# Optimization experiments

Hardware: AMD Instinct MI355X
Metric: run time of the kernel (lower is better)

Reference implementation:

```python
import jax, jax.numpy as jnp
import numpy as np

H_LSTM = 100
FORGET_BIAS = 1.0  # TF LSTMCell default


def conv2d(x, w, b, relu=True):
    # x: [N,H,W,Cin], w: [kh,kw,Cin,Cout]
    y = jax.lax.conv_general_dilated(
        x, w, window_strides=(1, 1), padding='SAME',
        dimension_numbers=('NHWC', 'HWIO', 'NHWC')) + b
    return jax.nn.relu(y) if relu else y


def lstm(xs, W, b):
    # xs: [T, N, D]; W: [D+H, 4H] with TF gate order (i, j, f, o); b: [4H]
    N = xs.shape[1]
    H = W.shape[1] // 4
    c0 = jnp.zeros((N, H), xs.dtype)
    h0 = jnp.zeros((N, H), xs.dtype)

    def step(carry, x_t):
        c, h = carry
        z = jnp.concatenate([x_t, h], axis=-1) @ W + b
        i, j, f, o = jnp.split(z, 4, axis=-1)
        c = jax.nn.sigmoid(f + FORGET_BIAS) * c + jax.nn.sigmoid(i) * jnp.tanh(j)
        h = jax.nn.sigmoid(o) * jnp.tanh(c)
        return (c, h), h

    _, hs = jax.lax.scan(step, (c0, h0), xs)
    return hs  # [T, N, H]


def setup_inputs() -> dict:
    B, L, C = 64, 55, 24
    key = jax.random.key(0)
    ks = jax.random.split(key, 32)
    s = 0.05
    inp = {'x': jax.random.normal(ks[0], (B, 13, 13, L, C), jnp.float32)}
    # 1x1 conv block (p1)
    cins = [C, 30, 30, 30]
    for i in range(4):
        inp[f'w1{i}'] = jax.random.normal(ks[1 + i], (1, 1, cins[i], 30), jnp.float32) * s
        inp[f'b1{i}'] = jnp.zeros((30,), jnp.float32)
    # 5x5 conv block (p2)
    for i in range(4):
        inp[f'w2{i}'] = jax.random.normal(ks[5 + i], (5, 5, 30, 30), jnp.float32) * s
        inp[f'b2{i}'] = jnp.zeros((30,), jnp.float32)
    # LSTM layers: inputs 30 -> 100 and 100 -> 100
    inp['lstm1_w'] = jax.random.uniform(ks[9], (30 + H_LSTM, 4 * H_LSTM), jnp.float32, -0.1, 0.1)
    inp['lstm1_b'] = jnp.zeros((4 * H_LSTM,), jnp.float32)
    inp['lstm2_w'] = jax.random.uniform(ks[10], (H_LSTM + H_LSTM, 4 * H_LSTM), jnp.float32, -0.1, 0.1)
    inp['lstm2_b'] = jnp.zeros((4 * H_LSTM,), jnp.float32)
    # final 1x1 conv, no activation
    inp['we'] = jax.random.normal(ks[11], (1, 1, H_LSTM, 1), jnp.float32) * s
    inp['be'] = jnp.zeros((1,), jnp.float32)
    return inp


def reference(x, w10, b10, w11, b11, w12, b12, w13, b13,
              w20, b20, w21, b21, w22, b22, w23, b23,
              lstm1_w, lstm1_b, lstm2_w, lstm2_b, we, be):
    B, _, _, L, C = x.shape
    # [B,13,13,L,C] -> [L,B,13,13,C] -> [L*B,13,13,C]
    h = jnp.transpose(x, (3, 0, 1, 2, 4)).reshape(L * B, 13, 13, C)
    for w, b in ((w10, b10), (w11, b11), (w12, b12), (w13, b13),
                 (w20, b20), (w21, b21), (w22, b22), (w23, b23)):
        h = conv2d(h, w, b, relu=True)
    # time-major sequence: [L, B*13*13, 30]
    h = h.reshape(L, B * 13 * 13, 30)
    h = lstm(h, lstm1_w, lstm1_b)
    h = lstm(h, lstm2_w, lstm2_b)
    h = h.reshape(L * B, 13, 13, H_LSTM)
    h = conv2d(h, we, be, relu=False)  # [L*B,13,13,1]
    h = h.reshape(L, B, 13, 13)
    return jnp.transpose(h, (1, 2, 3, 0))  # [B,13,13,L]
```

## Files before the change

kernel.cpp:

```cpp
#include <hip/hip_runtime.h>
#include <math.h>

#define N_ROWS 10816
#define T_SEQ 55
#define NPIX 169

__device__ __forceinline__ float fast_rcp(float x){
    return __builtin_amdgcn_rcpf(x);
}
__device__ __forceinline__ float fast_sig(float x){
    return fast_rcp(1.0f + __expf(-x));
}
__device__ __forceinline__ float fast_tanh(float x){
    float ax = fabsf(x);
    float e  = __expf(-2.0f*ax);
    float r  = (1.0f - e)*fast_rcp(1.0f + e);
    return copysignf(r, x);
}

typedef __attribute__((ext_vector_type(8))) _Float16 hfrag;
typedef __attribute__((ext_vector_type(4))) float facc;

__global__ __launch_bounds__(256) void repack_conv_f16(
    const float* __restrict__ w20, const float* __restrict__ w21,
    const float* __restrict__ w22, const float* __restrict__ w23,
    _Float16* __restrict__ cw)
{
    int i = blockIdx.x*256 + threadIdx.x;
    if (i >= 4*25600) return;
    int layer = i / 25600, r = i - layer*25600;
    int frag = r >> 9, e = r & 511;
    int kt = frag >> 1, ct = frag & 1;
    int lane = e >> 3, j = e & 7;
    int ci = ((lane>>4)<<3) + j;
    int co = ct*16 + (lane & 15);
    const float* w = (layer==0)?w20:(layer==1)?w21:(layer==2)?w22:w23;
    float v = (ci<30 && co<30) ? w[(size_t)(kt*30 + ci)*30 + co] : 0.f;
    cw[i] = (_Float16)v;
}

__global__ __launch_bounds__(256, 4) void conv_fused(
    const float* __restrict__ x,
    const float* __restrict__ w0, const float* __restrict__ b0,
    const float* __restrict__ w1, const float* __restrict__ b1,
    const float* __restrict__ w2, const float* __restrict__ b2,
    const float* __restrict__ w3, const float* __restrict__ b3,
    const _Float16* __restrict__ cw,
    const float* __restrict__ cb0, const float* __restrict__ cb1,
    const float* __restrict__ cb2, const float* __restrict__ cb3,
    float* __restrict__ buf)
{
    __shared__ __align__(16) _Float16 img[18*17*32];

    int bi = blockIdx.x;
    int l = bi >> 6, b = bi & 63;
    float* ip = buf + (size_t)l*30*N_ROWS + (size_t)b*NPIX;
    const int tid = threadIdx.x;
    const int wave = tid >> 6, lane = tid & 63;
    const int m16 = lane & 15, quad = lane >> 4;

    for (int i=tid; i<18*17*16; i+=256) ((unsigned*)img)[i] = 0u;
    __syncthreads();

    if (tid < NPIX){
        const float* xp = x + ((size_t)(b*NPIX + tid)*T_SEQ + l)*24;
        float in24[24];
        #pragma unroll
        for (int i=0;i<6;i++){
            float4 v = *(const float4*)(xp + 4*i);
            in24[4*i]=v.x; in24[4*i+1]=v.y; in24[4*i+2]=v.z; in24[4*i+3]=v.w;
        }
        float a[30], c[30];
        #pragma unroll
        for (int co=0;co<30;co++) a[co]=b0[co];
        #pragma unroll
        for (int ci=0;ci<24;ci++){
            float v = in24[ci];
            #pragma unroll
            for (int co=0;co<30;co++) a[co] = fmaf(v, w0[ci*30+co], a[co]);
        }
        #pragma unroll
        for (int co=0;co<30;co++) a[co] = fmaxf(a[co],0.f);

#define LAYER30(wp, bp) \
        { _Pragma("unroll") for (int co=0;co<30;co++) c[co]=(bp)[co]; \
          _Pragma("unroll") for (int ci=0;ci<30;ci++){ float v=a[ci]; \
            _Pragma("unroll") for (int co=0;co<30;co++) c[co]=fmaf(v,(wp)[ci*30+co],c[co]); } \
          _Pragma("unroll") for (int co=0;co<30;co++) a[co]=fmaxf(c[co],0.f); }

        LAYER30(w1,b1);
        LAYER30(w2,b2);
        LAYER30(w3,b3);
#undef LAYER30

        int py = tid/13, px = tid - py*13;
        int L = (py+2)*17 + (px+2);
        #pragma unroll
        for (int ci=0;ci<30;ci++)
            img[L*32 + ((((ci>>3) + L)&3)<<3) + (ci&7)] = (_Float16)a[ci];
    }

    int pL[3]; bool mv[3];
    #pragma unroll
    for (int mi=0; mi<3; mi++){
        int Mt = wave + mi*4;
        mv[mi] = (Mt < 11);
        int p = Mt*16 + m16;
        int py = p/13, px = p - py*13;
        pL[mi] = py*17 + px;
    }

    #pragma unroll 1
    for (int layer=0; layer<4; layer++){
        const float* bias = (layer==0)?cb0:(layer==1)?cb1:(layer==2)?cb2:cb3;
        const _Float16* wh = cw + (size_t)layer*25600;

        __syncthreads();

        float bb[2];
        #pragma unroll
        for (int nt=0; nt<2; nt++){
            int co = nt*16 + m16;
            bb[nt] = (co < 30) ? bias[co] : 0.f;
        }
        facc acc[3][2];
        #pragma unroll
        for (int mi=0; mi<3; mi++)
            #pragma unroll
            for (int nt=0; nt<2; nt++)
                acc[mi][nt] = (facc){bb[nt], bb[nt], bb[nt], bb[nt]};

        #pragma unroll 1
        for (int kt=0; kt<25; kt++){
            int dy = kt/5, dx = kt - dy*5;
            int Ld = dy*17 + dx;
            hfrag ah[3];
            #pragma unroll
            for (int mi=0; mi<3; mi++){
                if (mv[mi]){
                    int L = pL[mi] + Ld;
                    int o = L*32 + (((quad + L)&3)<<3);
                    ah[mi] = *(const hfrag*)(img + o);
                }
            }
            const _Float16* whp = wh + (size_t)(kt*2)*512 + lane*8;
            hfrag wh0 = *(const hfrag*)(whp);
            hfrag wh1 = *(const hfrag*)(whp + 512);
            #pragma unroll
            for (int mi=0; mi<3; mi++){
                if (mv[mi]){
                    acc[mi][0] = __builtin_amdgcn_mfma_f32_16x16x32_f16(ah[mi], wh0, acc[mi][0],0,0,0);
                    acc[mi][1] = __builtin_amdgcn_mfma_f32_16x16x32_f16(ah[mi], wh1, acc[mi][1],0,0,0);
                }
            }
        }

        __syncthreads();

        if (layer < 3){
            #pragma unroll
            for (int mi=0; mi<3; mi++){
                if (mv[mi]){
                    int Mt = wave + mi*4;
                    #pragma unroll
                    for (int nt=0; nt<2; nt++){
                        int co = nt*16 + m16;
                        if (co < 30){
                            #pragma unroll
                            for (int i2=0; i2<4; i2++){
                                int p = Mt*16 + quad*4 + i2;
                                if (p < NPIX){
                                    float v = fmaxf(acc[mi][nt][i2], 0.f);
                                    int py = p/13, px = p - py*13;
                                    int L = (py+2)*17 + (px+2);
                                    img[L*32 + ((((co>>3) + L)&3)<<3) + (co&7)] = (_Float16)v;
                                }
                            }
                        }
                    }
                }
            }
        } else {
            #pragma unroll
            for (int mi=0; mi<3; mi++){
                if (mv[mi]){
                    int Mt = wave + mi*4;
                    #pragma unroll
                    for (int nt=0; nt<2; nt++){
                        int co = nt*16 + m16;
                        if (co < 30){
                            #pragma unroll
                            for (int i2=0; i2<4; i2++){
                                int p = Mt*16 + quad*4 + i2;
                                if (p < NPIX)
                                    ip[(size_t)co*N_ROWS + p] = fmaxf(acc[mi][nt][i2], 0.f);
                            }
                        }
                    }
                }
            }
        }
    }
}

__global__ __launch_bounds__(256) void repack_mfma_f16(
    const float* __restrict__ l1w, const float* __restrict__ l1b,
    const float* __restrict__ l2w, const float* __restrict__ l2b,
    _Float16* __restrict__ bw1, _Float16* __restrict__ bw2,
    float* __restrict__ pbias1, float* __restrict__ pbias2)
{
    const int S1 = 5*32*512;
    const int S2 = 7*32*512;
    int i = blockIdx.x*256 + threadIdx.x;
    if (i < S1){
        int fr = i >> 9, r = i & 511;
        int kt = fr >> 5, ct = fr & 31;
        int lane = r >> 3, j = r & 7;
        int k = kt*32 + ((lane>>4)<<3) + j;
        int n = lane & 15;
        int cell = ((ct>>2)<<4) + n, g = ct & 3;
        float w = (k<130 && cell<100) ? l1w[(size_t)k*400 + g*100 + cell] : 0.f;
        bw1[i] = (_Float16)w;
    } else if (i < S1 + S2){
        int ii = i - S1;
        int fr = ii >> 9, r = ii & 511;
        int kt = fr >> 5, ct = fr & 31;
        int lane = r >> 3, j = r & 7;
        int k = kt*32 + ((lane>>4)<<3) + j;
        int n = lane & 15;
        int cell = ((ct>>2)<<4) + n, g = ct & 3;
        float w = (k<200 && cell<100) ? l2w[(size_t)k*400 + g*100 + cell] : 0.f;
        bw2[ii] = (_Float16)w;
    } else if (i < S1+S2+512){
        int col = i - S1 - S2;
        int ct = col >> 4, n = col & 15;
        int cell = ((ct>>2)<<4) + n, g = ct & 3;
        pbias1[col] = (cell<100) ? l1b[g*100+cell] : 0.f;
    } else if (i < S1+S2+1024){
        int col = i - S1 - S2 - 512;
        int ct = col >> 4, n = col & 15;
        int cell = ((ct>>2)<<4) + n, g = ct & 3;
        pbias2[col] = (cell<100) ? l2b[g*100+cell] : 0.f;
    }
}

#define NKT1 5
#define NKT2 7
#define M_BLK 32
#define RSTR 40
#define KTSTR (32*RSTR)
__global__ __launch_bounds__(512, 4) void lstm_mfma11(
    const float* __restrict__ xall,
    const _Float16* __restrict__ bw1, const _Float16* __restrict__ bw2,
    const float* __restrict__ pbias1, const float* __restrict__ pbias2,
    const float* __restrict__ we, const float* __restrict__ be,
    float* __restrict__ out)
{
    __shared__ __align__(16) _Float16 A1[NKT1*KTSTR];
    __shared__ __align__(16) _Float16 A2[NKT2*KTSTR];
    __shared__ float pbuf[8*M_BLK];

    const int tid  = threadIdx.x;
    const int w    = tid >> 6, lane = tid & 63;
    const int m16  = lane & 15, quad = lane >> 4;
    const int n0   = blockIdx.x * M_BLK;
    const int cell = w*16 + m16;
    const bool cv  = (cell < 100);

    for (int i=tid; i<NKT1*KTSTR; i+=512) A1[i]=(_Float16)0.f;
    for (int i=tid; i<NKT2*KTSTR; i+=512) A2[i]=(_Float16)0.f;
    for (int i=tid; i<8*M_BLK; i+=512) pbuf[i]=0.f;

    float cs1[2][4] = {{0,0,0,0},{0,0,0,0}};
    float cs2[2][4] = {{0,0,0,0},{0,0,0,0}};
    float b1[4], b2[4];
    #pragma unroll
    for (int g=0; g<4; g++){
        b1[g] = pbias1[(w*4+g)*16 + m16];
        b2[g] = pbias2[(w*4+g)*16 + m16];
    }
    const float weC = cv ? we[cell] : 0.f;
    const float be0 = be[0];

    const _Float16* w1p = bw1 + ((size_t)(w*4)*64 + lane)*8;
    const _Float16* w2p = bw2 + ((size_t)(w*4)*64 + lane)*8;

    const int sk = tid >> 3, sq = tid & 7;

    __syncthreads();

    if (tid < 240){
        float4 v = *(const float4*)(xall + (size_t)sk*N_ROWS + n0 + sq*4);
        A1[(sq*4+0)*RSTR + sk] = (_Float16)v.x;
        A1[(sq*4+1)*RSTR + sk] = (_Float16)v.y;
        A1[(sq*4+2)*RSTR + sk] = (_Float16)v.z;
        A1[(sq*4+3)*RSTR + sk] = (_Float16)v.w;
    }
    __syncthreads();

    facc acc[2][4];

#define GEMM(W0, NKT, AH, BI) \
    { _Pragma("unroll") \
      for (int mt=0; mt<2; mt++) \
        _Pragma("unroll") \
        for (int g=0; g<4; g++){ float bb=(BI)[g]; acc[mt][g]=(facc){bb,bb,bb,bb}; } \
      _Pragma("unroll 1") \
      for (int kt=0; kt<(NKT); kt++){ \
        hfrag ah[2]; \
        _Pragma("unroll") \
        for (int mt=0; mt<2; mt++){ \
            int off = kt*KTSTR + (mt*16+m16)*RSTR + (quad<<3); \
            ah[mt] = *(const hfrag*)((AH) + off); } \
        const _Float16* whp = (W0) + (size_t)kt*16384; \
        hfrag wh[4]; \
        _Pragma("unroll") \
        for (int g=0; g<4; g++) wh[g] = *(const hfrag*)(whp + (size_t)g*512); \
        _Pragma("unroll") \
        for (int g=0; g<4; g++){ \
            acc[0][g]=__builtin_amdgcn_mfma_f32_16x16x32_f16(ah[0],wh[g],acc[0][g],0,0,0); \
            acc[1][g]=__builtin_amdgcn_mfma_f32_16x16x32_f16(ah[1],wh[g],acc[1][g],0,0,0); } \
      } }

    for (int t=0; t<T_SEQ; t++){
        float4 xn;
        if (t+1 < T_SEQ && tid < 240)
            xn = *(const float4*)(xall + ((size_t)(t+1)*30+sk)*N_ROWS + n0 + sq*4);

        GEMM(w1p, NKT1, A1, b1);
        __syncthreads();

        if (cv){
            #pragma unroll
            for (int mt=0; mt<2; mt++){
                #pragma unroll
                for (int i2=0;i2<4;i2++){
                    float gi = fast_sig(acc[mt][0][i2]);
                    float gj = fast_tanh(acc[mt][1][i2]);
                    float gf = fast_sig(acc[mt][2][i2] + 1.0f);
                    float go = fast_sig(acc[mt][3][i2]);
                    float cn = gf*cs1[mt][i2] + gi*gj;
                    cs1[mt][i2] = cn;
                    float h = go*fast_tanh(cn);
                    int row = mt*16 + quad*4 + i2;
                    _Float16 hh = (_Float16)h;
                    int k1 = 30 + cell;
                    A1[(k1>>5)*KTSTR + row*RSTR + (k1&31)] = hh;
                    A2[(cell>>5)*KTSTR + row*RSTR + (cell&31)] = hh;
                }
            }
        }
        if (t+1 < T_SEQ && tid < 240){
            A1[(sq*4+0)*RSTR + sk] = (_Float16)xn.x;
            A1[(sq*4+1)*RSTR + sk] = (_Float16)xn.y;
            A1[(sq*4+2)*RSTR + sk] = (_Float16)xn.z;
            A1[(sq*4+3)*RSTR + sk] = (_Float16)xn.w;
        }
        __syncthreads();

        GEMM(w2p, NKT2, A2, b2);
        __syncthreads();

        if (w < 7){
            float pp[2][4] = {{0,0,0,0},{0,0,0,0}};
            if (cv){
                #pragma unroll
                for (int mt=0; mt<2; mt++){
                    #pragma unroll
                    for (int i2=0;i2<4;i2++){
                        float gi = fast_sig(acc[mt][0][i2]);
                        float gj = fast_tanh(acc[mt][1][i2]);
                        float gf = fast_sig(acc[mt][2][i2] + 1.0f);
                        float go = fast_sig(acc[mt][3][i2]);
                        float cn = gf*cs2[mt][i2] + gi*gj;
                        cs2[mt][i2] = cn;
                        float h = go*fast_tanh(cn);
                        pp[mt][i2] = h*weC;
                        int row = mt*16 + quad*4 + i2;
                        int k1 = 100 + cell;
                        A2[(k1>>5)*KTSTR + row*RSTR + (k1&31)] = (_Float16)h;
                    }
                }
            }
            #pragma unroll
            for (int mt=0; mt<2; mt++){
                #pragma unroll
                for (int i2=0;i2<4;i2++){
                    float p = pp[mt][i2];
                    p += __shfl_xor(p, 1);
                    p += __shfl_xor(p, 2);
                    p += __shfl_xor(p, 4);
                    p += __shfl_xor(p, 8);
                    pp[mt][i2] = p;
                }
            }
            if (m16 == 0){
                #pragma unroll
                for (int mt=0; mt<2; mt++)
                    #pragma unroll
                    for (int i2=0;i2<4;i2++)
                        pbuf[w*M_BLK + mt*16 + quad*4 + i2] = pp[mt][i2];
            }
        }
        __syncthreads();

        if (tid < M_BLK){
            float s = be0;
            #pragma unroll
            for (int ww=0; ww<8; ww++) s += pbuf[ww*M_BLK + tid];
            out[(size_t)(n0+tid)*T_SEQ + t] = s;
        }
    }
#undef GEMM
}

extern "C" void kernel_launch(void* const* d_in, const int* in_sizes, int n_in,
                              void* d_out, int out_size, void* d_ws, size_t ws_size,
                              hipStream_t stream)
{
    const float* x    = (const float*)d_in[0];
    const float* w10  = (const float*)d_in[1];  const float* b10 = (const float*)d_in[2];
    const float* w11  = (const float*)d_in[3];  const float* b11 = (const float*)d_in[4];
    const float* w12  = (const float*)d_in[5];  const float* b12 = (const float*)d_in[6];
    const float* w13  = (const float*)d_in[7];  const float* b13 = (const float*)d_in[8];
    const float* w20  = (const float*)d_in[9];  const float* b20 = (const float*)d_in[10];
    const float* w21  = (const float*)d_in[11]; const float* b21 = (const float*)d_in[12];
    const float* w22  = (const float*)d_in[13]; const float* b22 = (const float*)d_in[14];
    const float* w23  = (const float*)d_in[15]; const float* b23 = (const float*)d_in[16];
    const float* l1w  = (const float*)d_in[17]; const float* l1b = (const float*)d_in[18];
    const float* l2w  = (const float*)d_in[19]; const float* l2b = (const float*)d_in[20];
    const float* we   = (const float*)d_in[21]; const float* be  = (const float*)d_in[22];
    float* out = (float*)d_out;

    const size_t NF = (size_t)30*N_ROWS;
    float* buf0 = (float*)d_ws;
    unsigned short* packbase = (unsigned short*)(buf0 + (size_t)T_SEQ*NF);
    _Float16* bw1 = (_Float16*)packbase;
    _Float16* bw2 = (_Float16*)(packbase + 2*(5*32*512));
    float* pbias1 = (float*)(packbase + 2*(5*32*512) + 2*(7*32*512));
    float* pbias2 = pbias1 + 512;

    _Float16* cwf = (_Float16*)packbase;

    repack_conv_f16<<<(4*25600+255)/256, 256, 0, stream>>>(w20, w21, w22, w23, cwf);

    conv_fused<<<T_SEQ*64, 256, 0, stream>>>(
        x, w10,b10, w11,b11, w12,b12, w13,b13,
        cwf, b20, b21, b22, b23, buf0);

    const int REPACK_N = 5*32*512 + 7*32*512 + 1024;
    repack_mfma_f16<<<(REPACK_N+255)/256, 256, 0, stream>>>(
        l1w, l1b, l2w, l2b, bw1, bw2, pbias1, pbias2);

    lstm_mfma11<<<N_ROWS/M_BLK, 512, 0, stream>>>(buf0, bw1, bw2,
                                                  pbias1, pbias2, we, be, out);
}
```

Before: 886.9 us.

## Skew LSTM layers so layer-2 step t overlaps layer-1 step t+1

The LSTM loop is software-pipelined across the two layers. Each iteration now applies layer-1 step t and layer-2 step t-1, then runs the layer-2 GEMM for step t and the layer-1 GEMM for step t+1 back-to-back between the same pair of barriers, keeping two separate accumulator sets. This cuts the barriers per timestep from four to two and lets the two independent GEMMs interleave, with a prologue and epilogue to fill and drain the pipeline. The cost is higher register pressure from the second accumulator set, which could reduce occupancy under the launch bounds.

After: 923.8 us. +4.2%, slower.

```diff
diff --git a/kernel.cpp b/kernel.cpp
--- a/kernel.cpp
+++ b/kernel.cpp
@@ -249,7 +249,7 @@
 #define M_BLK 32
 #define RSTR 40
 #define KTSTR (32*RSTR)
-__global__ __launch_bounds__(512, 4) void lstm_mfma11(
+__global__ __launch_bounds__(512, 4) void lstm_mfma12(
     const float* __restrict__ xall,
     const _Float16* __restrict__ bw1, const _Float16* __restrict__ bw2,
     const float* __restrict__ pbias1, const float* __restrict__ pbias2,
@@ -298,13 +298,14 @@
     }
     __syncthreads();
 
-    facc acc[2][4];
-
-#define GEMM(W0, NKT, AH, BI) \
+    facc accA[2][4], accB[2][4];
+    float4 xn;
+
+#define GEMM(W0, NKT, AH, BI, ACC) \
     { _Pragma("unroll") \
       for (int mt=0; mt<2; mt++) \
         _Pragma("unroll") \
-        for (int g=0; g<4; g++){ float bb=(BI)[g]; acc[mt][g]=(facc){bb,bb,bb,bb}; } \
+        for (int g=0; g<4; g++){ float bb=(BI)[g]; (ACC)[mt][g]=(facc){bb,bb,bb,bb}; } \
       _Pragma("unroll 1") \
       for (int kt=0; kt<(NKT); kt++){ \
         hfrag ah[2]; \
@@ -318,27 +319,25 @@
         for (int g=0; g<4; g++) wh[g] = *(const hfrag*)(whp + (size_t)g*512); \
         _Pragma("unroll") \
         for (int g=0; g<4; g++){ \
-            acc[0][g]=__builtin_amdgcn_mfma_f32_16x16x32_f16(ah[0],wh[g],acc[0][g],0,0,0); \
-            acc[1][g]=__builtin_amdgcn_mfma_f32_16x16x32_f16(ah[1],wh[g],acc[1][g],0,0,0); } \
+            (ACC)[0][g]=__builtin_amdgcn_mfma_f32_16x16x32_f16(ah[0],wh[g],(ACC)[0][g],0,0,0); \
+            (ACC)[1][g]=__builtin_amdgcn_mfma_f32_16x16x32_f16(ah[1],wh[g],(ACC)[1][g],0,0,0); } \
       } }
 
+    GEMM(w1p, NKT1, A1, b1, accA);
+    if (tid < 240)
+        xn = *(const float4*)(xall + ((size_t)1*30+sk)*N_ROWS + n0 + sq*4);
+    __syncthreads();
+
     for (int t=0; t<T_SEQ; t++){
-        float4 xn;
-        if (t+1 < T_SEQ && tid < 240)
-            xn = *(const float4*)(xall + ((size_t)(t+1)*30+sk)*N_ROWS + n0 + sq*4);
-
-        GEMM(w1p, NKT1, A1, b1);
-        __syncthreads();
-
         if (cv){
             #pragma unroll
             for (int mt=0; mt<2; mt++){
                 #pragma unroll
                 for (int i2=0;i2<4;i2++){
-                    float gi = fast_sig(acc[mt][0][i2]);
-                    float gj = fast_tanh(acc[mt][1][i2]);
-                    float gf = fast_sig(acc[mt][2][i2] + 1.0f);
-                    float go = fast_sig(acc[mt][3][i2]);
+                    float gi = fast_sig(accA[mt][0][i2]);
+                    float gj = fast_tanh(accA[mt][1][i2]);
+                    float gf = fast_sig(accA[mt][2][i2] + 1.0f);
+                    float go = fast_sig(accA[mt][3][i2]);
                     float cn = gf*cs1[mt][i2] + gi*gj;
                     cs1[mt][i2] = cn;
                     float h = go*fast_tanh(cn);
@@ -350,28 +349,17 @@
                 }
             }
         }
-        if (t+1 < T_SEQ && tid < 240){
-            A1[(sq*4+0)*RSTR + sk] = (_Float16)xn.x;
-            A1[(sq*4+1)*RSTR + sk] = (_Float16)xn.y;
-            A1[(sq*4+2)*RSTR + sk] = (_Float16)xn.z;
-            A1[(sq*4+3)*RSTR + sk] = (_Float16)xn.w;
-        }
-        __syncthreads();
-
-        GEMM(w2p, NKT2, A2, b2);
-        __syncthreads();
-
-        if (w < 7){
+        if (t > 0 && w < 7){
             float pp[2][4] = {{0,0,0,0},{0,0,0,0}};
             if (cv){
                 #pragma unroll
                 for (int mt=0; mt<2; mt++){
                     #pragma unroll
                     for (int i2=0;i2<4;i2++){
-                        float gi = fast_sig(acc[mt][0][i2]);
-                        float gj = fast_tanh(acc[mt][1][i2]);
-                        float gf = fast_sig(acc[mt][2][i2] + 1.0f);
-                        float go = fast_sig(acc[mt][3][i2]);
+                        float gi = fast_sig(accB[mt][0][i2]);
+                        float gj = fast_tanh(accB[mt][1][i2]);
+                        float gf = fast_sig(accB[mt][2][i2] + 1.0f);
+                        float go = fast_sig(accB[mt][3][i2]);
                         float cn = gf*cs2[mt][i2] + gi*gj;
                         cs2[mt][i2] = cn;
                         float h = go*fast_tanh(cn);
@@ -402,14 +390,71 @@
                         pbuf[w*M_BLK + mt*16 + quad*4 + i2] = pp[mt][i2];
             }
         }
+        if (t+1 < T_SEQ && tid < 240){
+            A1[(sq*4+0)*RSTR + sk] = (_Float16)xn.x;
+            A1[(sq*4+1)*RSTR + sk] = (_Float16)xn.y;
+            A1[(sq*4+2)*RSTR + sk] = (_Float16)xn.z;
+            A1[(sq*4+3)*RSTR + sk] = (_Float16)xn.w;
+        }
         __syncthreads();
-
-        if (tid < M_BLK){
+        if (t > 0 && tid < M_BLK){
             float s = be0;
             #pragma unroll
             for (int ww=0; ww<8; ww++) s += pbuf[ww*M_BLK + tid];
-            out[(size_t)(n0+tid)*T_SEQ + t] = s;
-        }
+            out[(size_t)(n0+tid)*T_SEQ + (t-1)] = s;
+        }
+        GEMM(w2p, NKT2, A2, b2, accB);
+        if (t+1 < T_SEQ){
+            GEMM(w1p, NKT1, A1, b1, accA);
+            if (t+2 < T_SEQ && tid < 240)
+                xn = *(const float4*)(xall + ((size_t)(t+2)*30+sk)*N_ROWS + n0 + sq*4);
+        }
+        __syncthreads();
+    }
+
+    if (w < 7){
+        float pp[2][4] = {{0,0,0,0},{0,0,0,0}};
+        if (cv){
+            #pragma unroll
+            for (int mt=0; mt<2; mt++){
+                #pragma unroll
+                for (int i2=0;i2<4;i2++){
+                    float gi = fast_sig(accB[mt][0][i2]);
+                    float gj = fast_tanh(accB[mt][1][i2]);
+                    float gf = fast_sig(accB[mt][2][i2] + 1.0f);
+                    float go = fast_sig(accB[mt][3][i2]);
+                    float cn = gf*cs2[mt][i2] + gi*gj;
+                    float h = go*fast_tanh(cn);
+                    pp[mt][i2] = h*weC;
+                }
+            }
+        }
+        #pragma unroll
+        for (int mt=0; mt<2; mt++){
+            #pragma unroll
+            for (int i2=0;i2<4;i2++){
+                float p = pp[mt][i2];
+                p += __shfl_xor(p, 1);
+                p += __shfl_xor(p, 2);
+                p += __shfl_xor(p, 4);
+                p += __shfl_xor(p, 8);
+                pp[mt][i2] = p;
+            }
+        }
+        if (m16 == 0){
+            #pragma unroll
+            for (int mt=0; mt<2; mt++)
+                #pragma unroll
+                for (int i2=0;i2<4;i2++)
+                    pbuf[w*M_BLK + mt*16 + quad*4 + i2] = pp[mt][i2];
+        }
+    }
+    __syncthreads();
+    if (tid < M_BLK){
+        float s = be0;
+        #pragma unroll
+        for (int ww=0; ww<8; ww++) s += pbuf[ww*M_BLK + tid];
+        out[(size_t)(n0+tid)*T_SEQ + (T_SEQ-1)] = s;
     }
 #undef GEMM
 }
@@ -452,6 +497,6 @@
     repack_mfma_f16<<<(REPACK_N+255)/256, 256, 0, stream>>>(
         l1w, l1b, l2w, l2b, bw1, bw2, pbias1, pbias2);
 
-    lstm_mfma11<<<N_ROWS/M_BLK, 512, 0, stream>>>(buf0, bw1, bw2,
+    lstm_mfma12<<<N_ROWS/M_BLK, 512, 0, stream>>>(buf0, bw1, bw2,
                                                   pbias1, pbias2, we, be, out);
 }
```
